# Kernel tuning notes

Hardware: AMD Instinct MI355X
Metric: run time of the kernel (lower is better)

Reference implementation:

```python
import jax, jax.numpy as jnp
import numpy as np

B, S, D, H, HD, W, DFF = 2, 8192, 768, 12, 64, 256, 3072
NEG = -1e9


def ln(x, s, b, eps):
    m = jnp.mean(x, axis=-1, keepdims=True)
    v = jnp.mean((x - m) ** 2, axis=-1, keepdims=True)
    return (x - m) / jnp.sqrt(v + eps) * s + b


def band_attn(q, k, v, w):
    # q,k,v: [B,H,S,HD]; q already scaled by 1/sqrt(HD).
    b, h, s, d = q.shape
    nc = s // w  # non-overlapping query chunks of size w
    qc = q.reshape(b, h, nc, w, d)
    pad = ((0, 0), (0, 0), (w, w), (0, 0))
    kp = jnp.pad(k, pad)
    vp = jnp.pad(v, pad)
    # key chunk c covers global positions [c*w - w, c*w + 2w) -> length 3w
    idx = jnp.arange(nc)[:, None] * w + jnp.arange(3 * w)[None, :]  # [nc,3w]
    kc = kp[:, :, idx]  # [B,H,nc,3w,HD]
    vc = vp[:, :, idx]
    scores = jnp.einsum('bhcqd,bhckd->bhcqk', qc, kc)  # [B,H,nc,w,3w]
    # relative offset key-query: key global = c*w - w + j, query global = c*w + i
    rel = jnp.arange(3 * w)[None, :] - w - jnp.arange(w)[:, None]  # [w,3w]
    band = jnp.abs(rel) <= w
    kpos = jnp.arange(nc)[:, None] * w - w + jnp.arange(3 * w)[None, :]  # [nc,3w]
    valid = (kpos >= 0) & (kpos < s)
    mask = band[None, :, :] & valid[:, None, :]  # [nc,w,3w]
    scores = jnp.where(mask, scores, NEG)
    probs = jax.nn.softmax(scores, axis=-1)
    out = jnp.einsum('bhcqk,bhckd->bhcqd', probs, vc)
    return out.reshape(b, h, s, d)


def longformer_layer(hidden, pos_emb, tt_emb, emb_ln_s, emb_ln_b,
                     wq, bq, wk, bk, wv, bv, wo, bo, attn_ln_s, attn_ln_b,
                     wi, bi, wo2, bo2, out_ln_s, out_ln_b):
    # embeddings: inputs_embeds + position + token_type(0), LN eps 1e-12
    h = ln(hidden + pos_emb[None, :hidden.shape[1]] + tt_emb, emb_ln_s, emb_ln_b, 1e-12)
    def heads(x):
        return x.reshape(B, S, H, HD).transpose(0, 2, 1, 3)
    q = heads(h @ wq + bq) / jnp.sqrt(jnp.float32(HD))
    k = heads(h @ wk + bk)
    v = heads(h @ wv + bv)
    a = band_attn(q, k, v, W)  # [B,H,S,HD]
    a = a.transpose(0, 2, 1, 3).reshape(B, S, D)
    h2 = ln(h + (a @ wo + bo), attn_ln_s, attn_ln_b, 1e-12)
    inter = jax.nn.gelu(h2 @ wi + bi, approximate=False)
    return ln(h2 + (inter @ wo2 + bo2), out_ln_s, out_ln_b, 1e-12)


def setup_inputs() -> dict:
    key = jax.random.key(0)
    ks = jax.random.split(key, 16)
    wn = lambda k, shp: jax.random.normal(k, shp, jnp.float32) * 0.02
    d = {
        'src': jax.random.normal(ks[0], (B, S, D), jnp.float32),
        'pos_emb': wn(ks[1], (S, D)),
        'tt_emb': wn(ks[2], (D,)),
        'emb_ln_s': jnp.ones((D,)), 'emb_ln_b': jnp.zeros((D,)),
        'wq': wn(ks[3], (D, D)), 'bq': jnp.zeros((D,)),
        'wk': wn(ks[4], (D, D)), 'bk': jnp.zeros((D,)),
        'wv': wn(ks[5], (D, D)), 'bv': jnp.zeros((D,)),
        'wo': wn(ks[6], (D, D)), 'bo': jnp.zeros((D,)),
        'attn_ln_s': jnp.ones((D,)), 'attn_ln_b': jnp.zeros((D,)),
        'wi': wn(ks[7], (D, DFF)), 'bi': jnp.zeros((DFF,)),
        'wo2': wn(ks[8], (DFF, D)), 'bo2': jnp.zeros((D,)),
        'out_ln_s': jnp.ones((D,)), 'out_ln_b': jnp.zeros((D,)),
        'n1_s': jnp.ones((D,)), 'n1_b': jnp.zeros((D,)),
        'n2_s': jnp.ones((D,)), 'n2_b': jnp.zeros((D,)),
        'w1': wn(ks[9], (D, DFF)), 'b1': jnp.zeros((DFF,)),
        'w2': wn(ks[10], (DFF, D)), 'b2': jnp.zeros((D,)),
    }
    return d


def reference(src, pos_emb, tt_emb, emb_ln_s, emb_ln_b, wq, bq, wk, bk, wv, bv,
              wo, bo, attn_ln_s, attn_ln_b, wi, bi, wo2, bo2, out_ln_s, out_ln_b,
              n1_s, n1_b, n2_s, n2_b, w1, b1, w2, b2):
    hidden = ln(src, n1_s, n1_b, 1e-5)
    out = longformer_layer(hidden, pos_emb, tt_emb, emb_ln_s, emb_ln_b,
                           wq, bq, wk, bk, wv, bv, wo, bo, attn_ln_s, attn_ln_b,
                           wi, bi, wo2, bo2, out_ln_s, out_ln_b)
    src2 = src + out  # dropout is identity in eval
    ff = jax.nn.relu(ln(src2, n2_s, n2_b, 1e-5) @ w1 + b1)
    ff = ff @ w2 + b2
    return src2 + ff
```

## Files before the change

### kernel.cpp

```cpp
#include <hip/hip_runtime.h>

#define SLEN 8192
#define BD   768
#define NH   12
#define NTOK 16384
#define HTOK 8192

typedef __bf16 bf16;
typedef __bf16 bf16x8 __attribute__((ext_vector_type(8)));
typedef float  floatx4 __attribute__((ext_vector_type(4)));

#define MFMA16(a, b, c) __builtin_amdgcn_mfma_f32_16x16x32_bf16((a), (b), (c), 0, 0, 0)

__device__ __forceinline__ int iclamp(int v, int lo, int hi) {
  return v < lo ? lo : (v > hi ? hi : v);
}

__device__ __forceinline__ void gl2lds16(const bf16* g, bf16* l) {
  __builtin_amdgcn_global_load_lds(
      (const __attribute__((address_space(1))) void*)g,
      (__attribute__((address_space(3))) void*)l,
      16, 0, 0);
}

__global__ __launch_bounds__(256) void k_prep_w(const float* __restrict__ W,
                                                bf16* __restrict__ Wt,
                                                int K, int N, float scale) {
  __shared__ float tile[32][33];
  const int tid = threadIdx.x;
  const int tx = tid & 31, ty = tid >> 5;
  const int n0 = blockIdx.x * 32, k0 = blockIdx.y * 32;
#pragma unroll
  for (int i = 0; i < 32; i += 8)
    tile[ty + i][tx] = W[(size_t)(k0 + ty + i) * N + n0 + tx];
  __syncthreads();
#pragma unroll
  for (int i = 0; i < 32; i += 8)
    Wt[(size_t)(n0 + ty + i) * K + k0 + tx] = (bf16)(tile[tx][ty + i] * scale);
}

__global__ void k_prep_qkv_bias(const float* __restrict__ bq, const float* __restrict__ bk,
                                const float* __restrict__ bv, float* __restrict__ out) {
  int i = blockIdx.x * 256 + threadIdx.x;
  if (i < 768) out[i] = bq[i] * 0.125f;
  else if (i < 1536) out[i] = bk[i - 768];
  else if (i < 2304) out[i] = bv[i - 1536];
}

__device__ __forceinline__ float block_sum768(float v, float* red) {
#pragma unroll
  for (int off = 32; off > 0; off >>= 1) v += __shfl_down(v, off);
  __syncthreads();
  if ((threadIdx.x & 63) == 0) red[threadIdx.x >> 6] = v;
  __syncthreads();
  return red[0] + red[1] + red[2] + red[3];
}

__global__ __launch_bounds__(256) void k_ln_ln_emb(const float* __restrict__ src,
    const float* __restrict__ pos, const float* __restrict__ tt,
    const float* __restrict__ s1, const float* __restrict__ b1,
    const float* __restrict__ s2, const float* __restrict__ b2,
    float* __restrict__ hf, bf16* __restrict__ hb) {
  __shared__ float red[4];
  const int tid = threadIdx.x;
  const size_t row = blockIdx.x;
  const int sp = blockIdx.x & (SLEN - 1);
  const float* x = src + row * BD;
  float v0 = x[tid], v1 = x[tid + 256], v2 = x[tid + 512];
  const float mean = block_sum768(v0 + v1 + v2, red) * (1.f / 768.f);
  v0 -= mean; v1 -= mean; v2 -= mean;
  const float var = block_sum768(v0 * v0 + v1 * v1 + v2 * v2, red) * (1.f / 768.f);
  const float rstd = rsqrtf(var + 1e-5f);
  const float* pr = pos + (size_t)sp * BD;
  float y0 = v0 * rstd * s1[tid]       + b1[tid]       + pr[tid]       + tt[tid];
  float y1 = v1 * rstd * s1[tid + 256] + b1[tid + 256] + pr[tid + 256] + tt[tid + 256];
  float y2 = v2 * rstd * s1[tid + 512] + b1[tid + 512] + pr[tid + 512] + tt[tid + 512];
  const float mean2 = block_sum768(y0 + y1 + y2, red) * (1.f / 768.f);
  y0 -= mean2; y1 -= mean2; y2 -= mean2;
  const float var2 = block_sum768(y0 * y0 + y1 * y1 + y2 * y2, red) * (1.f / 768.f);
  const float rstd2 = rsqrtf(var2 + 1e-12f);
  float o0 = y0 * rstd2 * s2[tid]       + b2[tid];
  float o1 = y1 * rstd2 * s2[tid + 256] + b2[tid + 256];
  float o2 = y2 * rstd2 * s2[tid + 512] + b2[tid + 512];
  float* hr = hf + row * BD;
  bf16* hbr = hb + row * BD;
  hr[tid] = o0; hr[tid + 256] = o1; hr[tid + 512] = o2;
  hbr[tid] = (bf16)o0; hbr[tid + 256] = (bf16)o1; hbr[tid + 512] = (bf16)o2;
}

__global__ __launch_bounds__(256) void k_ln(const float* __restrict__ x,
    const float* __restrict__ s, const float* __restrict__ b, float eps,
    float* __restrict__ of, bf16* __restrict__ ob) {
  __shared__ float red[4];
  const int tid = threadIdx.x;
  const size_t row = blockIdx.x;
  const float* xr = x + row * BD;
  float v0 = xr[tid], v1 = xr[tid + 256], v2 = xr[tid + 512];
  const float mean = block_sum768(v0 + v1 + v2, red) * (1.f / 768.f);
  v0 -= mean; v1 -= mean; v2 -= mean;
  const float var = block_sum768(v0 * v0 + v1 * v1 + v2 * v2, red) * (1.f / 768.f);
  const float rstd = rsqrtf(var + eps);
  float o0 = v0 * rstd * s[tid] + b[tid];
  float o1 = v1 * rstd * s[tid + 256] + b[tid + 256];
  float o2 = v2 * rstd * s[tid + 512] + b[tid + 512];
  float* ofr = of + row * BD; bf16* obr = ob + row * BD;
  ofr[tid] = o0; ofr[tid + 256] = o1; ofr[tid + 512] = o2;
  obr[tid] = (bf16)o0; obr[tid + 256] = (bf16)o1; obr[tid + 512] = (bf16)o2;
}

__global__ __launch_bounds__(256) void k_ln_add_ln(const float* __restrict__ y,
    const float* __restrict__ src,
    const float* __restrict__ so, const float* __restrict__ bo_,
    const float* __restrict__ s2, const float* __restrict__ b2,
    float* __restrict__ src2, bf16* __restrict__ tb) {
  __shared__ float red[4];
  const int tid = threadIdx.x;
  const size_t row = blockIdx.x;
  const float* xr = y + row * BD;
  float v0 = xr[tid], v1 = xr[tid + 256], v2 = xr[tid + 512];
  const float mean = block_sum768(v0 + v1 + v2, red) * (1.f / 768.f);
  v0 -= mean; v1 -= mean; v2 -= mean;
  const float var = block_sum768(v0 * v0 + v1 * v1 + v2 * v2, red) * (1.f / 768.f);
  const float rstd = rsqrtf(var + 1e-12f);
  const float* sr = src + row * BD;
  float u0 = sr[tid]       + v0 * rstd * so[tid]       + bo_[tid];
  float u1 = sr[tid + 256] + v1 * rstd * so[tid + 256] + bo_[tid + 256];
  float u2 = sr[tid + 512] + v2 * rstd * so[tid + 512] + bo_[tid + 512];
  float* s2r = src2 + row * BD;
  s2r[tid] = u0; s2r[tid + 256] = u1; s2r[tid + 512] = u2;
  const float mean2 = block_sum768(u0 + u1 + u2, red) * (1.f / 768.f);
  u0 -= mean2; u1 -= mean2; u2 -= mean2;
  const float var2 = block_sum768(u0 * u0 + u1 * u1 + u2 * u2, red) * (1.f / 768.f);
  const float rstd2 = rsqrtf(var2 + 1e-5f);
  bf16* tr = tb + row * BD;
  tr[tid]       = (bf16)(u0 * rstd2 * s2[tid]       + b2[tid]);
  tr[tid + 256] = (bf16)(u1 * rstd2 * s2[tid + 256] + b2[tid + 256]);
  tr[tid + 512] = (bf16)(u2 * rstd2 * s2[tid + 512] + b2[tid + 512]);
}

template <int BM, int MINW, int ACT, bool RES, bool OUTB>
__global__ __launch_bounds__(256, MINW) void k_gemm(const bf16* __restrict__ A,
                                                    const bf16* __restrict__ Bt,
                                                    const float* __restrict__ bias,
                                                    const float* __restrict__ resid,
                                                    float* __restrict__ Cf,
                                                    bf16* __restrict__ Cb,
                                                    int M, int N, int K) {
  __shared__ __align__(16) bf16 As[2][BM * 32];
  __shared__ __align__(16) bf16 Bs[2][128 * 32];
  constexpr int NJ = (BM == 128) ? 4 : 2;
  const int tid = threadIdx.x;
  const int lane = tid & 63, wave = tid >> 6;
  const int quad = lane >> 4, c = lane & 15;
  const int gx = gridDim.x;
  const int G  = gx * gridDim.y;
  const int bid = blockIdx.y * gx + blockIdx.x;
  const int wgid = (bid & 7) * (G >> 3) + (bid >> 3);
  const int bx = wgid % gx, by = wgid / gx;
  const int n0 = bx * 128, m0 = by * BM;

  const int wrb = (BM == 128) ? (wave >> 1) * 64 : 0;
  const int wcb = (BM == 128) ? (wave & 1) * 64 : wave * 32;

  const int srow = lane >> 2;
  const int gch  = (((lane & 3) ^ ((lane >> 3) & 3)) << 3);
  const bf16* gA0;
  const bf16* gA1 = nullptr;
  int ldsA0, ldsA1 = 0;
  if constexpr (BM == 128) {
    gA0 = A + (size_t)(m0 + wave * 32 + srow) * K + gch;
    gA1 = A + (size_t)(m0 + wave * 32 + 16 + srow) * K + gch;
    ldsA0 = wave * 1024; ldsA1 = wave * 1024 + 512;
  } else {
    gA0 = A + (size_t)(m0 + wave * 16 + srow) * K + gch;
    ldsA0 = wave * 512;
  }
  const bf16* gB0 = Bt + (size_t)(n0 + wave * 32 + srow) * K + gch;
  const bf16* gB1 = Bt + (size_t)(n0 + wave * 32 + 16 + srow) * K + gch;
  const int ldsB0 = wave * 1024, ldsB1 = wave * 1024 + 512;

  const int xorq = ((quad ^ ((c >> 1) & 3)) << 3);
  int aOff[4], bOff[NJ];
#pragma unroll
  for (int i = 0; i < 4; ++i) aOff[i] = (wrb + i * 16 + c) * 32 + xorq;
#pragma unroll
  for (int j = 0; j < NJ; ++j) bOff[j] = (wcb + j * 16 + c) * 32 + xorq;

  floatx4 acc[4][NJ];
#pragma unroll
  for (int i = 0; i < 4; ++i)
#pragma unroll
    for (int j = 0; j < NJ; ++j) acc[i][j] = floatx4{0.f, 0.f, 0.f, 0.f};

  auto stage = [&](int buf, int k0) {
    gl2lds16(gA0 + k0, &As[buf][ldsA0]);
    if constexpr (BM == 128) gl2lds16(gA1 + k0, &As[buf][ldsA1]);
    gl2lds16(gB0 + k0, &Bs[buf][ldsB0]);
    gl2lds16(gB1 + k0, &Bs[buf][ldsB1]);
  };

  stage(0, 0);
  int cur = 0;
  for (int k0 = 0; k0 < K; k0 += 32) {
    __syncthreads();
    if (k0 + 32 < K) stage(cur ^ 1, k0 + 32);
    bf16x8 af[4], bfv[NJ];
#pragma unroll
    for (int i = 0; i < 4; ++i) af[i] = *(const bf16x8*)(&As[cur][aOff[i]]);
#pragma unroll
    for (int j = 0; j < NJ; ++j) bfv[j] = *(const bf16x8*)(&Bs[cur][bOff[j]]);
#pragma unroll
    for (int i = 0; i < 4; ++i)
#pragma unroll
      for (int j = 0; j < NJ; ++j)
        acc[i][j] = MFMA16(af[i], bfv[j], acc[i][j]);
    cur ^= 1;
  }

  const int rbase = m0 + wrb + quad * 4;
  const int cbase = n0 + wcb + c;
#pragma unroll
  for (int i = 0; i < 4; ++i) {
#pragma unroll
    for (int j = 0; j < NJ; ++j) {
      const int col = cbase + j * 16;
      const float bc = bias[col];
#pragma unroll
      for (int r = 0; r < 4; ++r) {
        const int row = rbase + i * 16 + r;
        float v = acc[i][j][r] + bc;
        if (RES) v += resid[(size_t)row * N + col];
        if (ACT == 1) v = 0.5f * v * (1.f + erff(v * 0.70710678118654752f));
        if (ACT == 2) v = fmaxf(v, 0.f);
        if (OUTB) Cb[(size_t)row * N + col] = (bf16)v;
        else      Cf[(size_t)row * N + col] = v;
      }
    }
  }
  (void)M;
}

__global__ __launch_bounds__(256) void k_vtrans(const bf16* __restrict__ qkv_b, bf16* __restrict__ vt) {
  __shared__ bf16 tile[64][72];
  const int tid = threadIdx.x;
  const int blk = blockIdx.x;
  const int h  = blk >> 7;
  const int st = blk & 127;
  const int s0 = st * 64;
  {
    const int d = tid & 63, si4 = tid >> 6;
    const bf16* src = qkv_b + (size_t)s0 * 2304 + 1536 + h * 64 + d;
#pragma unroll
    for (int i = 0; i < 16; ++i) {
      int s = si4 * 16 + i;
      tile[s][d] = src[(size_t)s * 2304];
    }
  }
  __syncthreads();
  {
    const int s = tid & 63, di4 = tid >> 6;
#pragma unroll
    for (int i = 0; i < 16; ++i) {
      int d = di4 * 16 + i;
      vt[((size_t)(h * 64 + d)) * SLEN + s0 + s] = tile[s][d];
    }
  }
}

__global__ __launch_bounds__(256, 4) void k_attn(const bf16* __restrict__ qkv_b,
                                                 const bf16* __restrict__ vt,
                                                 bf16* __restrict__ aout_b) {
  __shared__ __align__(16) bf16 Ks[2][64 * 64];
  __shared__ __align__(16) bf16 Vs[2][64 * 64];
  __shared__ __align__(16) bf16 Ps[4][16 * 64];
  const int tid  = threadIdx.x;
  const int wave = tid >> 6, lane = tid & 63;
  const int quad = lane >> 4, c = lane & 15;
  const int blk0 = blockIdx.x;
  const int wg   = ((blk0 & 7) * 192) + (blk0 >> 3);
  const int h    = wg >> 7;
  const int st   = wg & 127;
  const int q0b  = st * 64;
  const int q0   = q0b + wave * 16;

  const bf16* qp = qkv_b + (size_t)(q0 + c) * 2304 + h * 64 + quad * 8;
  const bf16x8 aq0 = *(const bf16x8*)(qp);
  const bf16x8 aq1 = *(const bf16x8*)(qp + 32);

  const int srow  = lane >> 3;
  const int chunk = ((lane & 7) ^ srow) << 3;
  const int krow0 = wave * 16 + srow;

  const int xlo = (quad ^ (c & 7)) << 3;
  const int xhi = ((quad + 4) ^ (c & 7)) << 3;

  floatx4 o[4];
  float m[4], l[4];
#pragma unroll
  for (int r = 0; r < 4; ++r) {
    o[r] = floatx4{0.f, 0.f, 0.f, 0.f};
    m[r] = -1e30f; l[r] = 0.f;
  }
  bf16* Pw = &Ps[wave][0];

  const int t_lo = st < 4 ? 4 - st : 0;
  const int t_hi = st > 123 ? 132 - st : 9;

  auto stage = [&](int buf, int t) {
    const int kb  = q0b - 256 + 64 * t;
    const int kr0 = iclamp(kb + krow0, 0, SLEN - 1);
    const int kr1 = iclamp(kb + krow0 + 8, 0, SLEN - 1);
    gl2lds16(qkv_b + (size_t)kr0 * 2304 + 768 + h * 64 + chunk, &Ks[buf][wave * 1024]);
    gl2lds16(qkv_b + (size_t)kr1 * 2304 + 768 + h * 64 + chunk, &Ks[buf][wave * 1024 + 512]);
    const int kbc = iclamp(kb, 0, SLEN - 64);
    gl2lds16(vt + (size_t)(h * 64 + krow0) * SLEN + kbc + chunk, &Vs[buf][wave * 1024]);
    gl2lds16(vt + (size_t)(h * 64 + krow0 + 8) * SLEN + kbc + chunk, &Vs[buf][wave * 1024 + 512]);
  };

  int cur = 0;
  stage(0, t_lo);
  for (int t = t_lo; t < t_hi; ++t) {
    __syncthreads();
    if (t + 1 < t_hi) stage(cur ^ 1, t + 1);
    const int kb = q0b - 256 + 64 * t;
    const bf16* Kb = &Ks[cur][0];
    const bf16* Vb = &Vs[cur][0];

    floatx4 s[4];
#pragma unroll
    for (int i = 0; i < 4; ++i) s[i] = floatx4{0.f, 0.f, 0.f, 0.f};
#pragma unroll
    for (int ks = 0; ks < 4; ++ks) {
      const bf16* kr = Kb + (ks * 16 + c) * 64;
      s[ks] = MFMA16(aq0, *(const bf16x8*)(kr + xlo), s[ks]);
      s[ks] = MFMA16(aq1, *(const bf16x8*)(kr + xhi), s[ks]);
    }
    if (t == 0 || t == 8) {
#pragma unroll
      for (int ks = 0; ks < 4; ++ks)
#pragma unroll
        for (int r = 0; r < 4; ++r) {
          int d = (kb + ks * 16 + c) - (q0 + quad * 4 + r);
          d = d < 0 ? -d : d;
          if (d > 256) s[ks][r] = -INFINITY;
        }
    }

    float tm[4], rs[4];
#pragma unroll
    for (int r = 0; r < 4; ++r)
      tm[r] = fmaxf(fmaxf(s[0][r], s[1][r]), fmaxf(s[2][r], s[3][r]));
#pragma unroll
    for (int off = 1; off < 16; off <<= 1)
#pragma unroll
      for (int r = 0; r < 4; ++r) tm[r] = fmaxf(tm[r], __shfl_xor(tm[r], off));
#pragma unroll
    for (int r = 0; r < 4; ++r) {
      const float mn = fmaxf(m[r], tm[r]);
      const float al = __expf(m[r] - mn);
      m[r] = mn;
      float sum = 0.f;
#pragma unroll
      for (int ks = 0; ks < 4; ++ks) { s[ks][r] = __expf(s[ks][r] - mn); sum += s[ks][r]; }
      rs[r] = sum;
      l[r] *= al;
#pragma unroll
      for (int n = 0; n < 4; ++n) o[n][r] *= al;
    }
#pragma unroll
    for (int off = 1; off < 16; off <<= 1)
#pragma unroll
      for (int r = 0; r < 4; ++r) rs[r] += __shfl_xor(rs[r], off);
#pragma unroll
    for (int r = 0; r < 4; ++r) l[r] += rs[r];

#pragma unroll
    for (int ks = 0; ks < 4; ++ks)
#pragma unroll
      for (int r = 0; r < 4; ++r) {
        const int prow = quad * 4 + r;
        const int col  = ks * 16 + c;
        Pw[prow * 64 + ((((col >> 3) ^ (prow & 7)) << 3) | (col & 7))] = (bf16)s[ks][r];
      }
    asm volatile("s_waitcnt lgkmcnt(0)" ::: "memory");
    const bf16x8 pa0 = *(const bf16x8*)(Pw + c * 64 + xlo);
    const bf16x8 pa1 = *(const bf16x8*)(Pw + c * 64 + xhi);
#pragma unroll
    for (int n = 0; n < 4; ++n) {
      const bf16* vr = Vb + (n * 16 + c) * 64;
      o[n] = MFMA16(pa0, *(const bf16x8*)(vr + xlo), o[n]);
      o[n] = MFMA16(pa1, *(const bf16x8*)(vr + xhi), o[n]);
    }
    cur ^= 1;
  }

#pragma unroll
  for (int r = 0; r < 4; ++r) {
    const float inv = 1.f / l[r];
    const size_t orow = (size_t)(q0 + quad * 4 + r) * BD + h * 64;
#pragma unroll
    for (int n = 0; n < 4; ++n)
      aout_b[orow + n * 16 + c] = (bf16)(o[n][r] * inv);
  }
}

extern "C" void kernel_launch(void* const* d_in, const int* in_sizes, int n_in,
                              void* d_out, int out_size, void* d_ws, size_t ws_size,
                              hipStream_t stream) {
  (void)in_sizes; (void)n_in; (void)out_size; (void)ws_size;
  const float* src     = (const float*)d_in[0];
  const float* pos_emb = (const float*)d_in[1];
  const float* tt_emb  = (const float*)d_in[2];
  const float* emb_s   = (const float*)d_in[3];
  const float* emb_b   = (const float*)d_in[4];
  const float* wq      = (const float*)d_in[5];
  const float* bq      = (const float*)d_in[6];
  const float* wk      = (const float*)d_in[7];
  const float* bk      = (const float*)d_in[8];
  const float* wv      = (const float*)d_in[9];
  const float* bv      = (const float*)d_in[10];
  const float* wo      = (const float*)d_in[11];
  const float* bo      = (const float*)d_in[12];
  const float* atn_s   = (const float*)d_in[13];
  const float* atn_b   = (const float*)d_in[14];
  const float* wi      = (const float*)d_in[15];
  const float* bi      = (const float*)d_in[16];
  const float* wo2     = (const float*)d_in[17];
  const float* bo2     = (const float*)d_in[18];
  const float* out_s   = (const float*)d_in[19];
  const float* out_b   = (const float*)d_in[20];
  const float* n1_s    = (const float*)d_in[21];
  const float* n1_b    = (const float*)d_in[22];
  const float* n2_s    = (const float*)d_in[23];
  const float* n2_b    = (const float*)d_in[24];
  const float* w1      = (const float*)d_in[25];
  const float* b1      = (const float*)d_in[26];
  const float* w2      = (const float*)d_in[27];
  const float* b2      = (const float*)d_in[28];

  char* ws = (char*)d_ws;
  size_t off = 0;
  auto alloc = [&](size_t bytes) {
    char* p = ws + off;
    off += (bytes + 255) & ~(size_t)255;
    return p;
  };

  bf16* qkvt  = (bf16*)alloc((size_t)2304 * 768 * 2);
  bf16* wot   = (bf16*)alloc((size_t)768 * 768 * 2);
  bf16* wit   = (bf16*)alloc((size_t)3072 * 768 * 2);
  bf16* wo2t  = (bf16*)alloc((size_t)768 * 3072 * 2);
  bf16* w1t   = (bf16*)alloc((size_t)3072 * 768 * 2);
  bf16* w2t   = (bf16*)alloc((size_t)768 * 3072 * 2);
  float* qkvb = (float*)alloc((size_t)2304 * 4);
  char* R1 = alloc((size_t)NTOK * BD * 4);
  char* R2 = alloc((size_t)NTOK * BD * 2);
  char* R3 = alloc((size_t)HTOK * 2304 * 2
                 + (size_t)NH * 64 * SLEN * 2
                 + (size_t)HTOK * BD * 2);

  float* h_f   = (float*)R1;
  bf16*  hb    = (bf16*)R2;
  bf16*  qkvB  = (bf16*)R3;
  bf16*  vtB   = (bf16*)(R3 + (size_t)HTOK * 2304 * 2);
  bf16*  aoutB = (bf16*)(R3 + (size_t)HTOK * 2304 * 2 + (size_t)NH * 64 * SLEN * 2);
  float* y1    = (float*)d_out;
  float* h2f   = (float*)R1;
  bf16*  h2b   = (bf16*)R2;
  bf16*  interC= (bf16*)R3;
  float* y2    = (float*)d_out;
  float* src2  = (float*)R1;
  bf16*  tb    = (bf16*)R2;
  bf16*  ff1C  = (bf16*)R3;
  float* outp  = (float*)d_out;

  dim3 blk(256);
  k_prep_w<<<dim3(24, 24), blk, 0, stream>>>(wq, qkvt,                 768, 768, 0.125f);
  k_prep_w<<<dim3(24, 24), blk, 0, stream>>>(wk, qkvt + 768 * 768,     768, 768, 1.f);
  k_prep_w<<<dim3(24, 24), blk, 0, stream>>>(wv, qkvt + 2 * 768 * 768, 768, 768, 1.f);
  k_prep_w<<<dim3(24, 24), blk, 0, stream>>>(wo, wot,                  768, 768, 1.f);
  k_prep_w<<<dim3(96, 24), blk, 0, stream>>>(wi, wit,    768, 3072, 1.f);
  k_prep_w<<<dim3(24, 96), blk, 0, stream>>>(wo2, wo2t, 3072, 768,  1.f);
  k_prep_w<<<dim3(96, 24), blk, 0, stream>>>(w1, w1t,    768, 3072, 1.f);
  k_prep_w<<<dim3(24, 96), blk, 0, stream>>>(w2, w2t,   3072, 768,  1.f);
  k_prep_qkv_bias<<<dim3(9), blk, 0, stream>>>(bq, bk, bv, qkvb);

  k_ln_ln_emb<<<dim3(NTOK), blk, 0, stream>>>(src, pos_emb, tt_emb, n1_s, n1_b,
                                              emb_s, emb_b, h_f, hb);
  for (int b = 0; b < 2; ++b) {
    const size_t tok0 = (size_t)b * HTOK;
    k_gemm<128, 2, 0, false, true><<<dim3(18, 64), blk, 0, stream>>>(
        hb + tok0 * BD, qkvt, qkvb, nullptr, nullptr, qkvB, HTOK, 2304, 768);
    k_vtrans<<<dim3(NH * 128), blk, 0, stream>>>(qkvB, vtB);
    k_attn<<<dim3(NH * 128), blk, 0, stream>>>(qkvB, vtB, aoutB);
    k_gemm<64, 4, 0, true, false><<<dim3(6, 128), blk, 0, stream>>>(
        aoutB, wot, bo, h_f + tok0 * BD, y1 + tok0 * BD, nullptr, HTOK, 768, 768);
  }
  k_ln<<<dim3(NTOK), blk, 0, stream>>>(y1, atn_s, atn_b, 1e-12f, h2f, h2b);
  for (int cchunk = 0; cchunk < 2; ++cchunk) {
    const size_t tok0 = (size_t)cchunk * HTOK;
    k_gemm<128, 2, 1, false, true><<<dim3(24, 64), blk, 0, stream>>>(
        h2b + tok0 * BD, wit, bi, nullptr, nullptr, interC, HTOK, 3072, 768);
    k_gemm<64, 4, 0, true, false><<<dim3(6, 128), blk, 0, stream>>>(
        interC, wo2t, bo2, h2f + tok0 * BD, y2 + tok0 * BD, nullptr, HTOK, 768, 3072);
  }
  k_ln_add_ln<<<dim3(NTOK), blk, 0, stream>>>(y2, src, out_s, out_b, n2_s, n2_b, src2, tb);
  for (int cchunk = 0; cchunk < 2; ++cchunk) {
    const size_t tok0 = (size_t)cchunk * HTOK;
    k_gemm<128, 2, 2, false, true><<<dim3(24, 64), blk, 0, stream>>>(
        tb + tok0 * BD, w1t, b1, nullptr, nullptr, ff1C, HTOK, 3072, 768);
    k_gemm<64, 4, 0, true, false><<<dim3(6, 128), blk, 0, stream>>>(
        ff1C, w2t, b2, src2 + tok0 * BD, outp + tok0 * BD, nullptr, HTOK, 768, 3072);
  }
}
```

Baseline: 1.052 ms.

## Deepen GEMM LDS pipeline to four stages with manual vmcnt waits

Replaces the double-buffered GEMM main loop with a four-slot LDS ring that keeps three 32-wide K slices in flight. Each step waits on explicit s_waitcnt vmcnt counts and a raw s_barrier instead of __syncthreads, and raises wave priority around the MFMA block. The aim is to hide global-to-LDS latency better and cut barrier stalls. The cost is double the LDS footprint, which lowers occupancy, so the BM=64 launch bound minimum drops from 4 to 3. The hand-counted waits are fragile and assume K is a multiple of 64.

```diff
diff --git a/kernel.cpp b/kernel.cpp
--- a/kernel.cpp
+++ b/kernel.cpp
@@ -11,6 +11,7 @@
 typedef float  floatx4 __attribute__((ext_vector_type(4)));
 
 #define MFMA16(a, b, c) __builtin_amdgcn_mfma_f32_16x16x32_bf16((a), (b), (c), 0, 0, 0)
+#define VMW(N) asm volatile("s_waitcnt vmcnt(" #N ")" ::: "memory")
 
 __device__ __forceinline__ int iclamp(int v, int lo, int hi) {
   return v < lo ? lo : (v > hi ? hi : v);
@@ -146,8 +147,8 @@
                                                     float* __restrict__ Cf,
                                                     bf16* __restrict__ Cb,
                                                     int M, int N, int K) {
-  __shared__ __align__(16) bf16 As[2][BM * 32];
-  __shared__ __align__(16) bf16 Bs[2][128 * 32];
+  __shared__ __align__(16) bf16 As[4][BM * 32];
+  __shared__ __align__(16) bf16 Bs[4][128 * 32];
   constexpr int NJ = (BM == 128) ? 4 : 2;
   const int tid = threadIdx.x;
   const int lane = tid & 63, wave = tid >> 6;
@@ -164,20 +165,21 @@
 
   const int srow = lane >> 2;
   const int gch  = (((lane & 3) ^ ((lane >> 3) & 3)) << 3);
+
   const bf16* gA0;
   const bf16* gA1 = nullptr;
-  int ldsA0, ldsA1 = 0;
+  int ldA0, ldA1 = 0;
   if constexpr (BM == 128) {
     gA0 = A + (size_t)(m0 + wave * 32 + srow) * K + gch;
     gA1 = A + (size_t)(m0 + wave * 32 + 16 + srow) * K + gch;
-    ldsA0 = wave * 1024; ldsA1 = wave * 1024 + 512;
+    ldA0 = (wave * 32) * 32; ldA1 = (wave * 32 + 16) * 32;
   } else {
     gA0 = A + (size_t)(m0 + wave * 16 + srow) * K + gch;
-    ldsA0 = wave * 512;
+    ldA0 = (wave * 16) * 32;
   }
   const bf16* gB0 = Bt + (size_t)(n0 + wave * 32 + srow) * K + gch;
   const bf16* gB1 = Bt + (size_t)(n0 + wave * 32 + 16 + srow) * K + gch;
-  const int ldsB0 = wave * 1024, ldsB1 = wave * 1024 + 512;
+  const int ldB0 = (wave * 32) * 32, ldB1 = (wave * 32 + 16) * 32;
 
   const int xorq = ((quad ^ ((c >> 1) & 3)) << 3);
   int aOff[4], bOff[NJ];
@@ -192,29 +194,47 @@
 #pragma unroll
     for (int j = 0; j < NJ; ++j) acc[i][j] = floatx4{0.f, 0.f, 0.f, 0.f};
 
-  auto stage = [&](int buf, int k0) {
-    gl2lds16(gA0 + k0, &As[buf][ldsA0]);
-    if constexpr (BM == 128) gl2lds16(gA1 + k0, &As[buf][ldsA1]);
-    gl2lds16(gB0 + k0, &Bs[buf][ldsB0]);
-    gl2lds16(gB1 + k0, &Bs[buf][ldsB1]);
+  auto batch = [&](int rb, int kg) {
+    gl2lds16(gA0 + kg, &As[rb][ldA0]);
+    if constexpr (BM == 128) gl2lds16(gA1 + kg, &As[rb][ldA1]);
+    gl2lds16(gB0 + kg, &Bs[rb][ldB0]);
+    gl2lds16(gB1 + kg, &Bs[rb][ldB1]);
   };
 
-  stage(0, 0);
-  int cur = 0;
-  for (int k0 = 0; k0 < K; k0 += 32) {
-    __syncthreads();
-    if (k0 + 32 < K) stage(cur ^ 1, k0 + 32);
+  auto compute_slice = [&](int rb) {
     bf16x8 af[4], bfv[NJ];
 #pragma unroll
-    for (int i = 0; i < 4; ++i) af[i] = *(const bf16x8*)(&As[cur][aOff[i]]);
-#pragma unroll
-    for (int j = 0; j < NJ; ++j) bfv[j] = *(const bf16x8*)(&Bs[cur][bOff[j]]);
+    for (int i = 0; i < 4; ++i) af[i] = *(const bf16x8*)(&As[rb][aOff[i]]);
+#pragma unroll
+    for (int j = 0; j < NJ; ++j) bfv[j] = *(const bf16x8*)(&Bs[rb][bOff[j]]);
+    __builtin_amdgcn_s_setprio(1);
 #pragma unroll
     for (int i = 0; i < 4; ++i)
 #pragma unroll
       for (int j = 0; j < NJ; ++j)
         acc[i][j] = MFMA16(af[i], bfv[j], acc[i][j]);
-    cur ^= 1;
+    __builtin_amdgcn_s_setprio(0);
+  };
+
+  const int nt = K >> 6;
+  batch(0, 0);
+  batch(1, 32);
+  batch(2, 64);
+  for (int t = 0; t < nt; ++t) {
+    const int b = t & 1;
+    const int kg = t << 6;
+    if (t < nt - 1) { if constexpr (BM == 128) VMW(8); else VMW(6); }
+    else            { if constexpr (BM == 128) VMW(4); else VMW(3); }
+    __builtin_amdgcn_sched_barrier(0);
+    asm volatile("s_barrier" ::: "memory");
+    if (t + 1 < nt) batch(((b ^ 1) << 1) | 1, kg + 96);
+    compute_slice(b << 1);
+    if (t < nt - 1) { if constexpr (BM == 128) VMW(8); else VMW(6); }
+    else            { VMW(0); }
+    __builtin_amdgcn_sched_barrier(0);
+    asm volatile("s_barrier" ::: "memory");
+    if (t + 2 < nt) batch(b << 1, kg + 128);
+    compute_slice((b << 1) | 1);
   }
 
   const int rbase = m0 + wrb + quad * 4;
@@ -493,7 +513,7 @@
         hb + tok0 * BD, qkvt, qkvb, nullptr, nullptr, qkvB, HTOK, 2304, 768);
     k_vtrans<<<dim3(NH * 128), blk, 0, stream>>>(qkvB, vtB);
     k_attn<<<dim3(NH * 128), blk, 0, stream>>>(qkvB, vtB, aoutB);
-    k_gemm<64, 4, 0, true, false><<<dim3(6, 128), blk, 0, stream>>>(
+    k_gemm<64, 3, 0, true, false><<<dim3(6, 128), blk, 0, stream>>>(
         aoutB, wot, bo, h_f + tok0 * BD, y1 + tok0 * BD, nullptr, HTOK, 768, 768);
   }
   k_ln<<<dim3(NTOK), blk, 0, stream>>>(y1, atn_s, atn_b, 1e-12f, h2f, h2b);
@@ -501,7 +521,7 @@
     const size_t tok0 = (size_t)cchunk * HTOK;
     k_gemm<128, 2, 1, false, true><<<dim3(24, 64), blk, 0, stream>>>(
         h2b + tok0 * BD, wit, bi, nullptr, nullptr, interC, HTOK, 3072, 768);
-    k_gemm<64, 4, 0, true, false><<<dim3(6, 128), blk, 0, stream>>>(
+    k_gemm<64, 3, 0, true, false><<<dim3(6, 128), blk, 0, stream>>>(
         interC, wo2t, bo2, h2f + tok0 * BD, y2 + tok0 * BD, nullptr, HTOK, 768, 3072);
   }
   k_ln_add_ln<<<dim3(NTOK), blk, 0, stream>>>(y2, src, out_s, out_b, n2_s, n2_b, src2, tb);
@@ -509,7 +529,7 @@
     const size_t tok0 = (size_t)cchunk * HTOK;
     k_gemm<128, 2, 2, false, true><<<dim3(24, 64), blk, 0, stream>>>(
         tb + tok0 * BD, w1t, b1, nullptr, nullptr, ff1C, HTOK, 3072, 768);
-    k_gemm<64, 4, 0, true, false><<<dim3(6, 128), blk, 0, stream>>>(
+    k_gemm<64, 3, 0, true, false><<<dim3(6, 128), blk, 0, stream>>>(
         ff1C, w2t, b2, src2 + tok0 * BD, outp + tok0 * BD, nullptr, HTOK, 768, 3072);
   }
 }
```

After: 1.109 ms. +5.4%, slower.
